# Kernel optimization log

Hardware: AMD Instinct MI355X
Metric: run time of the kernel (lower is better)

Reference implementation:

```python
import jax, jax.numpy as jnp
import numpy as np

B, S, D, H = 4, 2048, 1024, 16
DH = D // H


def setup_inputs() -> dict:
    key = jax.random.key(0)
    ks = jax.random.split(key, 12)
    std = 0.02
    return {
        "inputs": jax.random.normal(ks[0], (B, S, D), jnp.float32),
        "pre_block": jax.random.normal(ks[1], (B, S, D), jnp.float32),
        "ln_gamma": jnp.ones((D,), jnp.float32),
        "ln_beta": jnp.zeros((D,), jnp.float32),
        "Wq": jax.random.normal(ks[2], (D, D), jnp.float32) * std,
        "bq": jnp.zeros((D,), jnp.float32),
        "Wk": jax.random.normal(ks[3], (D, D), jnp.float32) * std,
        "bk": jnp.zeros((D,), jnp.float32),
        "Wv": jax.random.normal(ks[4], (D, D), jnp.float32) * std,
        "bv": jnp.zeros((D,), jnp.float32),
        "Wpos": jax.random.normal(ks[5], (D, D), jnp.float32) * std,
        "u_bias": jax.random.normal(ks[6], (H, DH), jnp.float32) * std,
        "v_bias": jax.random.normal(ks[7], (H, DH), jnp.float32) * std,
        "Wo": jax.random.normal(ks[8], (D, D), jnp.float32) * std,
        "bo": jnp.zeros((D,), jnp.float32),
    }


def _sinusoidal_pe(seq_len, d_model, dtype):
    pos = jnp.arange(seq_len, dtype=dtype)[:, None]                 # [S,1]
    i = jnp.arange(0, d_model, 2, dtype=dtype)
    div = jnp.exp(-(jnp.log(jnp.asarray(10000.0, dtype)) * i / d_model))  # [D/2]
    ang = pos * div                                                  # [S,D/2]
    pe = jnp.zeros((seq_len, d_model), dtype)
    pe = pe.at[:, 0::2].set(jnp.sin(ang)).at[:, 1::2].set(jnp.cos(ang))
    return pe


def _rel_shift(pos_score):
    # Transformer-XL style relative shift: pos_score [B,H,S,S]
    b, h, s1, s2 = pos_score.shape
    pad = jnp.zeros((b, h, s1, 1), pos_score.dtype)
    padded = jnp.concatenate([pad, pos_score], axis=-1)              # [B,H,S,S+1]
    padded = padded.reshape(b, h, s2 + 1, s1)
    return padded[:, :, 1:].reshape(b, h, s1, s2)


def _layer_norm(x, gamma, beta, eps=1e-5):
    mu = jnp.mean(x, axis=-1, keepdims=True)
    var = jnp.mean(jnp.square(x - mu), axis=-1, keepdims=True)
    return (x - mu) * jax.lax.rsqrt(var + eps) * gamma + beta


def reference(inputs, pre_block, ln_gamma, ln_beta, Wq, bq, Wk, bk, Wv, bv,
              Wpos, u_bias, v_bias, Wo, bo):
    b, s, d = inputs.shape
    h = u_bias.shape[0]
    dh = d // h

    pe = _sinusoidal_pe(s, d, inputs.dtype)                          # [S,D]
    x = _layer_norm(inputs, ln_gamma, ln_beta)

    q = (x @ Wq + bq).reshape(b, s, h, dh)
    k = (x @ Wk + bk).reshape(b, s, h, dh)
    v = (pre_block @ Wv + bv).reshape(b, s, h, dh)
    p = (pe @ Wpos).reshape(s, h, dh)                                # shared across batch

    content = jnp.einsum('bshd,bthd->bhst', q + u_bias, k)           # [B,H,S,S]
    pos_score = jnp.einsum('bshd,thd->bhst', q + v_bias, p)          # [B,H,S,S]
    pos_score = _rel_shift(pos_score)

    score = (content + pos_score) / jnp.sqrt(jnp.asarray(d, inputs.dtype))
    attn = jax.nn.softmax(score, axis=-1)
    ctx = jnp.einsum('bhst,bthd->bshd', attn, v).reshape(b, s, d)
    return ctx @ Wo + bo
```

## Files before the change

### kernel.cpp

```cpp
#include <hip/hip_runtime.h>
#include <hip/hip_bf16.h>
#include <cmath>

#define B_ 4
#define S_ 2048
#define D_ 1024
#define H_ 16
#define DH_ 64

typedef __attribute__((ext_vector_type(8))) short short8;
typedef __attribute__((ext_vector_type(4))) float f32x4;
#define MFMA_BF16(a, b, c) __builtin_amdgcn_mfma_f32_16x16x32_bf16(a, b, c, 0, 0, 0)

static __device__ __forceinline__ float b2f(unsigned short u) {
  union { unsigned int i; float f; } x; x.i = ((unsigned int)u) << 16; return x.f;
}
static __device__ __forceinline__ unsigned short f2b(float f) {
  union { float f; unsigned int i; } x; x.f = f;
  unsigned int r = x.i + 0x7FFFu + ((x.i >> 16) & 1u);
  return (unsigned short)(r >> 16);
}
static __device__ __forceinline__ unsigned int pk2(float a, float b) {
  __hip_bfloat162 h = __float22bfloat162_rn(make_float2(a, b));
  return *(unsigned int*)&h;
}
static __device__ __forceinline__ int mod96(int x) {
  int t = x >> 5;
  int q = (t * 43691) >> 17;
  int m3 = t - q * 3;
  return (x & 31) + (m3 << 5);
}
static __device__ __forceinline__ int clampS(int x) {
  return x < 0 ? 0 : (x > S_ - 1 ? S_ - 1 : x);
}
typedef __attribute__((address_space(3))) unsigned int lds_u32_t;
typedef __attribute__((address_space(1))) const unsigned int glb_u32_t;
static __device__ __forceinline__ void gload_lds16(const void* g, void* l) {
  __builtin_amdgcn_global_load_lds((glb_u32_t*)g, (lds_u32_t*)l, 16, 0, 0);
}

__global__ __launch_bounds__(256) void prep_kernel(
    const float* __restrict__ inputs, const float* __restrict__ gamma,
    const float* __restrict__ beta, unsigned short* __restrict__ xb,
    const float* __restrict__ pre, unsigned short* __restrict__ preb,
    const double* __restrict__ dt, unsigned short* __restrict__ pe,
    const float* __restrict__ Wq, unsigned short* __restrict__ wtq,
    const float* __restrict__ Wk, unsigned short* __restrict__ wtk,
    const float* __restrict__ Wv, unsigned short* __restrict__ wtv,
    const float* __restrict__ Wp, unsigned short* __restrict__ wtp,
    const float* __restrict__ Wo, unsigned short* __restrict__ wto) {
  __shared__ __align__(16) float shf[64 * 65];
  int bid = blockIdx.x;
  int tid = threadIdx.x;
  if (bid < 8192) {
    int row = bid;
    float4 val = ((const float4*)(inputs + (size_t)row * D_))[tid];
    float s = val.x + val.y + val.z + val.w;
    float sq = val.x * val.x + val.y * val.y + val.z * val.z + val.w * val.w;
#pragma unroll
    for (int o = 32; o > 0; o >>= 1) {
      s += __shfl_down(s, o);
      sq += __shfl_down(sq, o);
    }
    int wid = tid >> 6;
    if ((tid & 63) == 0) { shf[wid] = s; shf[4 + wid] = sq; }
    __syncthreads();
    if (tid == 0) {
      float ts = shf[0] + shf[1] + shf[2] + shf[3];
      float tq = shf[4] + shf[5] + shf[6] + shf[7];
      float mu = ts * (1.0f / D_);
      float var = tq * (1.0f / D_) - mu * mu;
      shf[8] = mu;
      shf[9] = rsqrtf(var + 1e-5f);
    }
    __syncthreads();
    float mu = shf[8], rs = shf[9];
    float4 g = ((const float4*)gamma)[tid];
    float4 be = ((const float4*)beta)[tid];
    ushort4 o;
    o.x = f2b((val.x - mu) * rs * g.x + be.x);
    o.y = f2b((val.y - mu) * rs * g.y + be.y);
    o.z = f2b((val.z - mu) * rs * g.z + be.z);
    o.w = f2b((val.w - mu) * rs * g.w + be.w);
    *(ushort4*)(xb + (size_t)row * D_ + tid * 4) = o;
    return;
  }
  bid -= 8192;
  if (bid < 8192) {
    size_t idx = (size_t)(bid * 256 + tid) * 4;
    float4 v = *(const float4*)(pre + idx);
    ushort4 o; o.x = f2b(v.x); o.y = f2b(v.y); o.z = f2b(v.z); o.w = f2b(v.w);
    *(ushort4*)(preb + idx) = o;
    return;
  }
  bid -= 8192;
  if (bid < 4096) {
    int idx = bid * 256 + tid;
    int t = idx >> 9;
    int i = idx & 511;
    double ang = (double)t * dt[i];
    double k = floor(ang * 0.15915494309189535);
    float red = (float)(ang - k * 6.283185307179586);
    ushort2 sc;
    sc.x = f2b(sinf(red));
    sc.y = f2b(cosf(red));
    *(ushort2*)(pe + (size_t)t * D_ + 2 * i) = sc;
    return;
  }
  bid -= 4096;
  const float* W; unsigned short* WT;
  switch (bid >> 8) {
    case 0: W = Wq; WT = wtq; break;
    case 1: W = Wk; WT = wtk; break;
    case 2: W = Wv; WT = wtv; break;
    case 3: W = Wp; WT = wtp; break;
    default: W = Wo; WT = wto; break;
  }
  int tile = bid & 255;
  int n0 = (tile & 15) * 64, k0 = (tile >> 4) * 64;
#pragma unroll
  for (int c = 0; c < 4; c++) {
    int idx = tid + c * 256;
    int r = idx >> 4;
    int ch = (idx & 15) * 4;
    float4 d = *(const float4*)(W + (size_t)(k0 + r) * D_ + n0 + ch);
    shf[r * 65 + ch] = d.x; shf[r * 65 + ch + 1] = d.y;
    shf[r * 65 + ch + 2] = d.z; shf[r * 65 + ch + 3] = d.w;
  }
  __syncthreads();
  {
    int n = tid >> 2;
    int ch = (tid & 3) * 16;
    unsigned short tmp[8];
#pragma unroll
    for (int half = 0; half < 2; half++) {
#pragma unroll
      for (int e = 0; e < 8; e++) tmp[e] = f2b(shf[(ch + half * 8 + e) * 65 + n]);
      *(short8*)(WT + (size_t)(n0 + n) * D_ + k0 + ch + half * 8) = *(short8*)tmp;
    }
  }
}

template <bool F32OUT>
__global__ __launch_bounds__(256) void gemm_bf16_t(const unsigned short* __restrict__ A,
                                                   const unsigned short* __restrict__ BT,
                                                   const float* __restrict__ bias,
                                                   void* __restrict__ Cv,
                                                   int M, int N, int K) {
  __shared__ __align__(16) unsigned short As[128 * 32];
  __shared__ __align__(16) unsigned short Bs[128 * 32];
  const int tid = threadIdx.x;
  const int wid = tid >> 6, lane = tid & 63, quad = lane >> 4, l15 = lane & 15;
  const int m0 = blockIdx.y * 128, n0 = blockIdx.x * 128;
  const int moff = (wid >> 1) * 64, noff = (wid & 1) * 64;
  f32x4 acc[4][4];
#pragma unroll
  for (int i = 0; i < 4; i++)
#pragma unroll
    for (int j = 0; j < 4; j++) acc[i][j] = (f32x4){0.f, 0.f, 0.f, 0.f};

  const int cb0 = wid * 64;
  const int c0 = cb0 + lane;
  const int r0 = c0 >> 2, ch0 = (c0 & 3) * 8;
  const int c1 = c0 + 256;
  const int r1 = c1 >> 2, ch1 = (c1 & 3) * 8;

  for (int k0 = 0; k0 < K; k0 += 32) {
    __syncthreads();
    gload_lds16(A + (size_t)(m0 + r0) * K + k0 + ch0, &As[cb0 * 8]);
    gload_lds16(BT + (size_t)(n0 + r0) * K + k0 + ch0, &Bs[cb0 * 8]);
    gload_lds16(A + (size_t)(m0 + r1) * K + k0 + ch1, &As[(cb0 + 256) * 8]);
    gload_lds16(BT + (size_t)(n0 + r1) * K + k0 + ch1, &Bs[(cb0 + 256) * 8]);
    __syncthreads();
    short8 af[4], bf[4];
#pragma unroll
    for (int i = 0; i < 4; i++)
      af[i] = *(const short8*)&As[(moff + i * 16 + l15) * 32 + quad * 8];
#pragma unroll
    for (int j = 0; j < 4; j++)
      bf[j] = *(const short8*)&Bs[(noff + j * 16 + l15) * 32 + quad * 8];
#pragma unroll
    for (int i = 0; i < 4; i++)
#pragma unroll
      for (int j = 0; j < 4; j++) acc[i][j] = MFMA_BF16(af[i], bf[j], acc[i][j]);
  }
#pragma unroll
  for (int i = 0; i < 4; i++) {
    int row = m0 + moff + i * 16 + quad * 4;
#pragma unroll
    for (int j = 0; j < 4; j++) {
      int col = n0 + noff + j * 16 + l15;
      float bb = bias ? bias[col] : 0.f;
#pragma unroll
      for (int g = 0; g < 4; g++) {
        if (F32OUT)
          ((float*)Cv)[(size_t)(row + g) * N + col] = acc[i][j][g] + bb;
        else
          ((unsigned short*)Cv)[(size_t)(row + g) * N + col] = f2b(acc[i][j][g] + bb);
      }
    }
  }
}

__global__ __launch_bounds__(256) void gemm_qk_bf16(const unsigned short* __restrict__ A,
                                                    const unsigned short* __restrict__ BT,
                                                    const float* __restrict__ bq,
                                                    const float* __restrict__ bk,
                                                    unsigned short* __restrict__ outQ,
                                                    unsigned short* __restrict__ outK) {
  const int K = D_;
  __shared__ __align__(16) unsigned short As[128 * 32];
  __shared__ __align__(16) unsigned short Bs[128 * 32];
  const int tid = threadIdx.x;
  const int wid = tid >> 6, lane = tid & 63, quad = lane >> 4, l15 = lane & 15;
  const int m0 = blockIdx.y * 128, n0 = blockIdx.x * 128;
  const int moff = (wid >> 1) * 64, noff = (wid & 1) * 64;
  f32x4 acc[4][4];
#pragma unroll
  for (int i = 0; i < 4; i++)
#pragma unroll
    for (int j = 0; j < 4; j++) acc[i][j] = (f32x4){0.f, 0.f, 0.f, 0.f};

  const int cb0 = wid * 64;
  const int c0 = cb0 + lane;
  const int r0 = c0 >> 2, ch0 = (c0 & 3) * 8;
  const int c1 = c0 + 256;
  const int r1 = c1 >> 2, ch1 = (c1 & 3) * 8;

  for (int k0 = 0; k0 < K; k0 += 32) {
    __syncthreads();
    gload_lds16(A + (size_t)(m0 + r0) * K + k0 + ch0, &As[cb0 * 8]);
    gload_lds16(BT + (size_t)(n0 + r0) * K + k0 + ch0, &Bs[cb0 * 8]);
    gload_lds16(A + (size_t)(m0 + r1) * K + k0 + ch1, &As[(cb0 + 256) * 8]);
    gload_lds16(BT + (size_t)(n0 + r1) * K + k0 + ch1, &Bs[(cb0 + 256) * 8]);
    __syncthreads();
    short8 af[4], bf[4];
#pragma unroll
    for (int i = 0; i < 4; i++)
      af[i] = *(const short8*)&As[(moff + i * 16 + l15) * 32 + quad * 8];
#pragma unroll
    for (int j = 0; j < 4; j++)
      bf[j] = *(const short8*)&Bs[(noff + j * 16 + l15) * 32 + quad * 8];
#pragma unroll
    for (int i = 0; i < 4; i++)
#pragma unroll
      for (int j = 0; j < 4; j++) acc[i][j] = MFMA_BF16(af[i], bf[j], acc[i][j]);
  }
  const float* bias = (n0 < D_) ? bq : bk;
  unsigned short* outp = (n0 < D_) ? outQ : outK;
  const int nn0 = n0 & (D_ - 1);
#pragma unroll
  for (int i = 0; i < 4; i++) {
    int row = m0 + moff + i * 16 + quad * 4;
#pragma unroll
    for (int j = 0; j < 4; j++) {
      int col = nn0 + noff + j * 16 + l15;
      float bb = bias[col];
#pragma unroll
      for (int g = 0; g < 4; g++)
        outp[(size_t)(row + g) * D_ + col] = f2b(acc[i][j][g] + bb);
    }
  }
}

__global__ __launch_bounds__(256) void post_kernel(const unsigned short* __restrict__ v,
                                                   unsigned short* __restrict__ vt,
                                                   const unsigned short* __restrict__ p,
                                                   const float* __restrict__ ub,
                                                   const float* __restrict__ vbb,
                                                   float* __restrict__ cw) {
  __shared__ __align__(16) unsigned short t[64 * 72];
  int bid = blockIdx.x;
  int tid = threadIdx.x;
  if (bid < 2048) {
    int s0 = (bid & 31) * 64, h = (bid >> 5) & 15, b = bid >> 9;
#pragma unroll
    for (int c = 0; c < 2; c++) {
      int idx = tid + c * 256;
      int r = idx >> 3, ch = (idx & 7) * 8;
      short8 d = *(const short8*)(v + (((size_t)b * S_ + s0 + r) * H_ + h) * DH_ + ch);
      *(short8*)&t[r * 72 + ch] = d;
    }
    __syncthreads();
    int dh = tid >> 2, ch = tid & 3;
    unsigned short tmp[8];
#pragma unroll
    for (int half = 0; half < 2; half++) {
#pragma unroll
      for (int e = 0; e < 8; e++) tmp[e] = t[(ch * 16 + half * 8 + e) * 72 + dh];
      *(short8*)(vt + ((size_t)(b * H_ + h) * 64 + dh) * S_ + s0 + ch * 16 + half * 8) =
          *(short8*)tmp;
    }
    return;
  }
  int idx = (bid - 2048) * 256 + tid;
  int r = idx & (S_ - 1), h = idx >> 11;
  float s = 0.f;
#pragma unroll 8
  for (int c = 0; c < 64; c++)
    s += (vbb[h * 64 + c] - ub[h * 64 + c]) * b2f(p[(size_t)r * D_ + h * 64 + c]);
  cw[idx] = s;
}

__global__ __launch_bounds__(256) void attn_kernel(const unsigned short* __restrict__ q,
                                                   const unsigned short* __restrict__ kg,
                                                   const unsigned short* __restrict__ vtg,
                                                   const unsigned short* __restrict__ pg,
                                                   const float* __restrict__ ub,
                                                   const float* __restrict__ cw,
                                                   unsigned short* __restrict__ ctx) {
  int flat = blockIdx.x + 32 * (blockIdx.y + 16 * blockIdx.z);
  int swz = (flat & 7) * 256 + (flat >> 3);
  const int i0 = (swz & 31) * 64;
  const int h = (swz >> 5) & 15;
  const int b = swz >> 9;
  const int tid = threadIdx.x;
  const int wid = tid >> 6, lane = tid & 63, quad = lane >> 4, l15 = lane & 15;
  const int wr0 = wid * 16;
  const int ib = i0 >> 5;

  __shared__ __align__(16) unsigned short ks[32 * 64];
  __shared__ __align__(16) unsigned short ps[2][32 * 64];
  __shared__ __align__(16) unsigned short vts[2][64 * 32];
  __shared__ __align__(16) unsigned short prb[64 * 40];
  __shared__ __align__(16) unsigned short bandA[64 * 100];
  __shared__ __align__(16) unsigned short bandB[64 * 100];

  const int srow = tid >> 3;
  const int lcS = ((tid & 7) ^ (srow & 7)) * 8;
  const int vrow = tid >> 2, vch = (tid & 3) * 8;
  const int pc0 = (quad ^ (l15 & 7)) * 8;

  const unsigned short* kgl = kg + ((size_t)b * S_ * H_ + h) * DH_ + lcS;
  const unsigned short* pgl = pg + h * 64 + lcS;
  const unsigned short* vgl = vtg + ((size_t)(b * H_ + h) * 64 + vrow) * S_ + vch;
  const float* cwh = cw + h * S_;
  const int wb = wid * 512;

  short8 qa00, qa01, qa10, qa11;
  {
    auto ldq = [&](int r, int c0) -> short8 {
      int qi = i0 + r; if (qi > S_ - 1) qi = S_ - 1;
      short8 raw = *(const short8*)(q + (((size_t)b * S_ + qi) * H_ + h) * DH_ + c0);
      unsigned short t[8];
#pragma unroll
      for (int e = 0; e < 8; e++)
        t[e] = f2b(b2f((unsigned short)raw[e]) + ub[h * 64 + c0 + e]);
      return *(short8*)t;
    };
    qa00 = ldq(wr0 + l15, quad * 8);
    qa01 = ldq(wr0 + l15, 32 + quad * 8);
    qa10 = ldq(wr0 + l15 + 1, quad * 8);
    qa11 = ldq(wr0 + l15 + 1, 32 + quad * 8);
  }

  const int brow = (wr0 + l15) * 100;

  auto band_compute = [&](const unsigned short* src, int w, int rhi) {
    int rbase = rhi - 31;
    short8 a0 = w ? qa10 : qa00;
    short8 a1 = w ? qa11 : qa01;
    unsigned short* band = w ? bandB : bandA;
    const int OFF = w ? 2 : 1;
#pragma unroll
    for (int ct = 0; ct < 2; ct++) {
      int ro = (ct * 16 + l15) * 64;
      short8 b0 = *(const short8*)&src[ro + pc0];
      short8 b1 = *(const short8*)&src[ro + (pc0 ^ 32)];
      f32x4 acc = (f32x4){0.f, 0.f, 0.f, 0.f};
      acc = MFMA_BF16(b0, a0, acc);
      acc = MFMA_BF16(b1, a1, acc);
      int r0 = rbase + ct * 16 + quad * 4;
      float c0 = cwh[clampS(r0)];
      float c1 = cwh[clampS(r0 + 1)];
      float c2 = cwh[clampS(r0 + 2)];
      float c3 = cwh[clampS(r0 + 3)];
      int col = mod96(r0 + 960 + OFF);
      uint2 pv = make_uint2(pk2(acc[0] + c0, acc[1] + c1), pk2(acc[2] + c2, acc[3] + c3));
      *(uint2*)&band[brow + col] = pv;
      if (col == 0) *(uint2*)&band[brow + 96] = pv;
    }
  };

  {
    const int TW[5] = {0, 0, 0, 1, 1};
    const int TR[5] = {S_ + 30 - i0 - 64, S_ + 30 - i0 - 32, S_ + 30 - i0, 29, 61};
    {
      int rc = clampS(TR[0] - 31 + srow);
      gload_lds16(pgl + (size_t)rc * D_, &ps[0][wb]);
      gload_lds16(kgl + (size_t)srow * (H_ * DH_), &ks[wb]);
      gload_lds16(vgl, &vts[0][wb]);
    }
    __syncthreads();
#pragma unroll
    for (int t = 0; t < 5; t++) {
      if (t < 4) {
        int rc = clampS(TR[t + 1] - 31 + srow);
        gload_lds16(pgl + (size_t)rc * D_, &ps[(t + 1) & 1][wb]);
      }
      band_compute(ps[t & 1], TW[t], TR[t]);
      __syncthreads();
    }
  }

  float lsum = 0.f;
  f32x4 Oa[4];
#pragma unroll
  for (int ct = 0; ct < 4; ct++) Oa[ct] = (f32x4){0.f, 0.f, 0.f, 0.f};

  int cA = mod96(S_ + quad * 4 - i0 - wr0 - l15);
  int cB = mod96(2112 + quad * 4 - i0 - wr0 - l15);
  int cwin = 0, crhi = 0, chave = 0;

  const float SCL = 0.03125f;
  const unsigned int prbw = (wr0 + l15) * 40 + quad * 4;

  for (int jt = 0; jt < 64; jt++) {
    const int j0 = jt * 32;
    const int cur = jt & 1, nxt = cur ^ 1;
    int pwin = 0, prhi = 0, havep = 0;
    {
      int j0x = j0 + 32;
      if (j0x <= i0 + 63) { pwin = 0; prhi = S_ + 30 - i0 + j0x; havep = 1; }
      else if (jt < 63)   { pwin = 1; prhi = j0x - i0 + 29;      havep = 1; }
      if (havep) {
        int rc = clampS(prhi - 31 + srow);
        gload_lds16(pgl + (size_t)rc * D_, &ps[nxt][wb]);
      }
      if (jt < 63)
        gload_lds16(vgl + (size_t)(j0 + 32), &vts[nxt][wb]);
    }
    if (chave) band_compute(ps[cur], cwin, crhi);
    f32x4 cc[2];
    {
#pragma unroll
      for (int ct = 0; ct < 2; ct++) {
        int ro = (ct * 16 + l15) * 64;
        short8 a0 = *(const short8*)&ks[ro + pc0];
        short8 a1 = *(const short8*)&ks[ro + (pc0 ^ 32)];
        f32x4 acc = (f32x4){0.f, 0.f, 0.f, 0.f};
        acc = MFMA_BF16(a0, qa00, acc);
        acc = MFMA_BF16(a1, qa01, acc);
        cc[ct] = acc;
      }
    }
    __syncthreads();
    if (jt < 63)
      gload_lds16(kgl + (size_t)(j0 + 32 + srow) * (H_ * DH_), &ks[wb]);
    if (jt < ib) {
#pragma unroll
      for (int ct = 0; ct < 2; ct++) {
        int c0 = ct ? (cA + 16 >= 96 ? cA + 16 - 96 : cA + 16) : cA;
        const unsigned short* base = &bandA[brow + c0];
        float e0 = __expf((cc[ct][0] + b2f(base[0])) * SCL);
        float e1 = __expf((cc[ct][1] + b2f(base[1])) * SCL);
        float e2 = __expf((cc[ct][2] + b2f(base[2])) * SCL);
        float e3 = __expf((cc[ct][3] + b2f(base[3])) * SCL);
        *(uint2*)&prb[prbw + ct * 16] = make_uint2(pk2(e0, e1), pk2(e2, e3));
        lsum += (e0 + e1) + (e2 + e3);
      }
    } else if (jt >= ib + 3) {
#pragma unroll
      for (int ct = 0; ct < 2; ct++) {
        int c0 = ct ? (cB + 16 >= 96 ? cB + 16 - 96 : cB + 16) : cB;
        const unsigned short* base = &bandB[brow + c0];
        float e0 = __expf((cc[ct][0] + b2f(base[0])) * SCL);
        float e1 = __expf((cc[ct][1] + b2f(base[1])) * SCL);
        float e2 = __expf((cc[ct][2] + b2f(base[2])) * SCL);
        float e3 = __expf((cc[ct][3] + b2f(base[3])) * SCL);
        *(uint2*)&prb[prbw + ct * 16] = make_uint2(pk2(e0, e1), pk2(e2, e3));
        lsum += (e0 + e1) + (e2 + e3);
      }
    } else {
#pragma unroll
      for (int ct = 0; ct < 2; ct++) {
        int jbase = j0 + ct * 16 + quad * 4;
        float ev[4];
#pragma unroll
        for (int g = 0; g < 4; g++) {
          int d = jbase + g - (i0 + wr0 + l15);
          float t;
          if (d == 1) t = 0.f;
          else if (d <= 0) t = b2f(bandA[brow + mod96(S_ + d)]);
          else t = b2f(bandB[brow + mod96(d)]);
          ev[g] = __expf((cc[ct][g] + t) * SCL);
          lsum += ev[g];
        }
        *(uint2*)&prb[prbw + ct * 16] = make_uint2(pk2(ev[0], ev[1]), pk2(ev[2], ev[3]));
      }
    }
    {
      short8 af = *(const short8*)&prb[(wr0 + l15) * 40 + quad * 8];
#pragma unroll
      for (int ct = 0; ct < 4; ct++) {
        short8 bf = *(const short8*)&vts[cur][(ct * 16 + l15) * 32 + quad * 8];
        Oa[ct] = MFMA_BF16(af, bf, Oa[ct]);
      }
    }
    __syncthreads();
    cwin = pwin; crhi = prhi; chave = havep;
    cA += 32; if (cA >= 96) cA -= 96;
    cB += 32; if (cB >= 96) cB -= 96;
  }
  float ltot = lsum;
  ltot += __shfl_xor(ltot, 16);
  ltot += __shfl_xor(ltot, 32);
#pragma unroll
  for (int g = 0; g < 4; g++) {
    float lg = __shfl(ltot, quad * 4 + g);
    float inv = 1.f / lg;
    int i = i0 + wr0 + quad * 4 + g;
    unsigned short* dst = ctx + ((size_t)b * S_ + i) * D_ + h * 64;
#pragma unroll
    for (int ct = 0; ct < 4; ct++) dst[ct * 16 + l15] = f2b(Oa[ct][g] * inv);
  }
}

extern "C" void kernel_launch(void* const* d_in, const int* in_sizes, int n_in,
                              void* d_out, int out_size, void* d_ws, size_t ws_size,
                              hipStream_t stream) {
  const float* inputs = (const float*)d_in[0];
  const float* pre_block = (const float*)d_in[1];
  const float* ln_gamma = (const float*)d_in[2];
  const float* ln_beta = (const float*)d_in[3];
  const float* Wq = (const float*)d_in[4];
  const float* bq = (const float*)d_in[5];
  const float* Wk = (const float*)d_in[6];
  const float* bk = (const float*)d_in[7];
  const float* Wv = (const float*)d_in[8];
  const float* bv = (const float*)d_in[9];
  const float* Wpos = (const float*)d_in[10];
  const float* u_bias = (const float*)d_in[11];
  const float* v_bias = (const float*)d_in[12];
  const float* Wo = (const float*)d_in[13];
  const float* bo = (const float*)d_in[14];
  float* out = (float*)d_out;

  char* ws = (char*)d_ws;
  const size_t NBS = (size_t)B_ * S_ * D_;
  unsigned short* xb = (unsigned short*)ws;
  unsigned short* ctx = (unsigned short*)ws;
  unsigned short* preb = (unsigned short*)(ws + NBS * 2);
  unsigned short* peb = (unsigned short*)(ws + NBS * 4);
  char* base = ws + NBS * 4 + (size_t)S_ * D_ * 2;
  unsigned short* wtq = (unsigned short*)(base);
  unsigned short* wtk = (unsigned short*)(base + (size_t)D_ * D_ * 2);
  unsigned short* wtv = (unsigned short*)(base + (size_t)D_ * D_ * 4);
  unsigned short* wtp = (unsigned short*)(base + (size_t)D_ * D_ * 6);
  unsigned short* wto = (unsigned short*)(base + (size_t)D_ * D_ * 8);
  unsigned short* qb = (unsigned short*)(base + (size_t)D_ * D_ * 10);
  unsigned short* kb = qb + NBS;
  unsigned short* vb = kb + NBS;
  unsigned short* vtb = vb + NBS;
  unsigned short* pb = vtb + NBS;
  float* cww = (float*)(pb + (size_t)S_ * D_);
  double* divtab = (double*)(cww + (size_t)H_ * S_);

  static double h_divtab[512];
  static bool h_init = false;
  if (!h_init) {
    for (int i = 0; i < 512; i++)
      h_divtab[i] = exp(-(log(10000.0) * (2.0 * i) / (double)D_));
    h_init = true;
  }
  hipMemcpyAsync(divtab, h_divtab, 512 * sizeof(double), hipMemcpyHostToDevice, stream);

  prep_kernel<<<21760, 256, 0, stream>>>(inputs, ln_gamma, ln_beta, xb,
                                         pre_block, preb, divtab, peb,
                                         Wq, wtq, Wk, wtk, Wv, wtv, Wpos, wtp, Wo, wto);
  gemm_qk_bf16<<<dim3(16, 64), 256, 0, stream>>>(xb, wtq, bq, bk, qb, kb);
  gemm_bf16_t<false><<<dim3(8, 64), 256, 0, stream>>>(preb, wtv, bv, vb, B_ * S_, D_, D_);
  gemm_bf16_t<false><<<dim3(8, 16), 256, 0, stream>>>(peb, wtp, nullptr, pb, S_, D_, D_);
  post_kernel<<<2176, 256, 0, stream>>>(vb, vtb, pb, u_bias, v_bias, cww);
  attn_kernel<<<dim3(32, 16, 4), 256, 0, stream>>>(qb, kb, vtb, pb, u_bias, cww, ctx);
  gemm_bf16_t<true><<<dim3(8, 64), 256, 0, stream>>>(ctx, wto, bo, out, B_ * S_, D_, D_);
}
```

Before: 635.1 us.

## Fold v_bias into a separate query copy instead of precomputed positional correction

Previously the query was biased by u_bias for both the content and positional MFMAs, and a correction term (v_bias-u_bias)·p was precomputed per head and row in post_kernel, then loaded and added in the band computation. Now the attention kernel keeps separate q+u_bias and q+v_bias register copies and uses the latter for the positional band, so the correction buffer, its computation blocks and its gathered loads go away. This costs extra registers for the additional query fragments. It also raises wave priority around the MFMA section with s_setprio.

```diff
diff --git a/kernel.cpp b/kernel.cpp
--- a/kernel.cpp
+++ b/kernel.cpp
@@ -264,42 +264,28 @@
 }
 
 __global__ __launch_bounds__(256) void post_kernel(const unsigned short* __restrict__ v,
-                                                   unsigned short* __restrict__ vt,
-                                                   const unsigned short* __restrict__ p,
-                                                   const float* __restrict__ ub,
-                                                   const float* __restrict__ vbb,
-                                                   float* __restrict__ cw) {
+                                                   unsigned short* __restrict__ vt) {
   __shared__ __align__(16) unsigned short t[64 * 72];
   int bid = blockIdx.x;
   int tid = threadIdx.x;
-  if (bid < 2048) {
-    int s0 = (bid & 31) * 64, h = (bid >> 5) & 15, b = bid >> 9;
-#pragma unroll
-    for (int c = 0; c < 2; c++) {
-      int idx = tid + c * 256;
-      int r = idx >> 3, ch = (idx & 7) * 8;
-      short8 d = *(const short8*)(v + (((size_t)b * S_ + s0 + r) * H_ + h) * DH_ + ch);
-      *(short8*)&t[r * 72 + ch] = d;
-    }
-    __syncthreads();
-    int dh = tid >> 2, ch = tid & 3;
-    unsigned short tmp[8];
-#pragma unroll
-    for (int half = 0; half < 2; half++) {
-#pragma unroll
-      for (int e = 0; e < 8; e++) tmp[e] = t[(ch * 16 + half * 8 + e) * 72 + dh];
-      *(short8*)(vt + ((size_t)(b * H_ + h) * 64 + dh) * S_ + s0 + ch * 16 + half * 8) =
-          *(short8*)tmp;
-    }
-    return;
-  }
-  int idx = (bid - 2048) * 256 + tid;
-  int r = idx & (S_ - 1), h = idx >> 11;
-  float s = 0.f;
-#pragma unroll 8
-  for (int c = 0; c < 64; c++)
-    s += (vbb[h * 64 + c] - ub[h * 64 + c]) * b2f(p[(size_t)r * D_ + h * 64 + c]);
-  cw[idx] = s;
+  int s0 = (bid & 31) * 64, h = (bid >> 5) & 15, b = bid >> 9;
+#pragma unroll
+  for (int c = 0; c < 2; c++) {
+    int idx = tid + c * 256;
+    int r = idx >> 3, ch = (idx & 7) * 8;
+    short8 d = *(const short8*)(v + (((size_t)b * S_ + s0 + r) * H_ + h) * DH_ + ch);
+    *(short8*)&t[r * 72 + ch] = d;
+  }
+  __syncthreads();
+  int dh = tid >> 2, ch = tid & 3;
+  unsigned short tmp[8];
+#pragma unroll
+  for (int half = 0; half < 2; half++) {
+#pragma unroll
+    for (int e = 0; e < 8; e++) tmp[e] = t[(ch * 16 + half * 8 + e) * 72 + dh];
+    *(short8*)(vt + ((size_t)(b * H_ + h) * 64 + dh) * S_ + s0 + ch * 16 + half * 8) =
+        *(short8*)tmp;
+  }
 }
 
 __global__ __launch_bounds__(256) void attn_kernel(const unsigned short* __restrict__ q,
@@ -307,7 +293,7 @@
                                                    const unsigned short* __restrict__ vtg,
                                                    const unsigned short* __restrict__ pg,
                                                    const float* __restrict__ ub,
-                                                   const float* __restrict__ cw,
+                                                   const float* __restrict__ vbias,
                                                    unsigned short* __restrict__ ctx) {
   int flat = blockIdx.x + 32 * (blockIdx.y + 16 * blockIdx.z);
   int swz = (flat & 7) * 256 + (flat >> 3);
@@ -334,32 +320,44 @@
   const unsigned short* kgl = kg + ((size_t)b * S_ * H_ + h) * DH_ + lcS;
   const unsigned short* pgl = pg + h * 64 + lcS;
   const unsigned short* vgl = vtg + ((size_t)(b * H_ + h) * 64 + vrow) * S_ + vch;
-  const float* cwh = cw + h * S_;
   const int wb = wid * 512;
 
-  short8 qa00, qa01, qa10, qa11;
+  short8 qc0, qc1, qA0, qA1, qB0, qB1;
   {
-    auto ldq = [&](int r, int c0) -> short8 {
+    auto ldq2 = [&](int r, int c0, short8& outU, short8& outV) {
       int qi = i0 + r; if (qi > S_ - 1) qi = S_ - 1;
       short8 raw = *(const short8*)(q + (((size_t)b * S_ + qi) * H_ + h) * DH_ + c0);
-      unsigned short t[8];
+      unsigned short tu[8], tv[8];
+#pragma unroll
+      for (int e = 0; e < 8; e++) {
+        float f = b2f((unsigned short)raw[e]);
+        tu[e] = f2b(f + ub[h * 64 + c0 + e]);
+        tv[e] = f2b(f + vbias[h * 64 + c0 + e]);
+      }
+      outU = *(short8*)tu;
+      outV = *(short8*)tv;
+    };
+    auto ldqv = [&](int r, int c0) -> short8 {
+      int qi = i0 + r; if (qi > S_ - 1) qi = S_ - 1;
+      short8 raw = *(const short8*)(q + (((size_t)b * S_ + qi) * H_ + h) * DH_ + c0);
+      unsigned short tv[8];
 #pragma unroll
       for (int e = 0; e < 8; e++)
-        t[e] = f2b(b2f((unsigned short)raw[e]) + ub[h * 64 + c0 + e]);
-      return *(short8*)t;
+        tv[e] = f2b(b2f((unsigned short)raw[e]) + vbias[h * 64 + c0 + e]);
+      return *(short8*)tv;
     };
-    qa00 = ldq(wr0 + l15, quad * 8);
-    qa01 = ldq(wr0 + l15, 32 + quad * 8);
-    qa10 = ldq(wr0 + l15 + 1, quad * 8);
-    qa11 = ldq(wr0 + l15 + 1, 32 + quad * 8);
+    ldq2(wr0 + l15, quad * 8, qc0, qA0);
+    ldq2(wr0 + l15, 32 + quad * 8, qc1, qA1);
+    qB0 = ldqv(wr0 + l15 + 1, quad * 8);
+    qB1 = ldqv(wr0 + l15 + 1, 32 + quad * 8);
   }
 
   const int brow = (wr0 + l15) * 100;
 
   auto band_compute = [&](const unsigned short* src, int w, int rhi) {
     int rbase = rhi - 31;
-    short8 a0 = w ? qa10 : qa00;
-    short8 a1 = w ? qa11 : qa01;
+    short8 a0 = w ? qB0 : qA0;
+    short8 a1 = w ? qB1 : qA1;
     unsigned short* band = w ? bandB : bandA;
     const int OFF = w ? 2 : 1;
 #pragma unroll
@@ -371,12 +369,8 @@
       acc = MFMA_BF16(b0, a0, acc);
       acc = MFMA_BF16(b1, a1, acc);
       int r0 = rbase + ct * 16 + quad * 4;
-      float c0 = cwh[clampS(r0)];
-      float c1 = cwh[clampS(r0 + 1)];
-      float c2 = cwh[clampS(r0 + 2)];
-      float c3 = cwh[clampS(r0 + 3)];
       int col = mod96(r0 + 960 + OFF);
-      uint2 pv = make_uint2(pk2(acc[0] + c0, acc[1] + c1), pk2(acc[2] + c2, acc[3] + c3));
+      uint2 pv = make_uint2(pk2(acc[0], acc[1]), pk2(acc[2], acc[3]));
       *(uint2*)&band[brow + col] = pv;
       if (col == 0) *(uint2*)&band[brow + 96] = pv;
     }
@@ -430,6 +424,7 @@
       if (jt < 63)
         gload_lds16(vgl + (size_t)(j0 + 32), &vts[nxt][wb]);
     }
+    __builtin_amdgcn_s_setprio(1);
     if (chave) band_compute(ps[cur], cwin, crhi);
     f32x4 cc[2];
     {
@@ -439,11 +434,12 @@
         short8 a0 = *(const short8*)&ks[ro + pc0];
         short8 a1 = *(const short8*)&ks[ro + (pc0 ^ 32)];
         f32x4 acc = (f32x4){0.f, 0.f, 0.f, 0.f};
-        acc = MFMA_BF16(a0, qa00, acc);
-        acc = MFMA_BF16(a1, qa01, acc);
+        acc = MFMA_BF16(a0, qc0, acc);
+        acc = MFMA_BF16(a1, qc1, acc);
         cc[ct] = acc;
       }
     }
+    __builtin_amdgcn_s_setprio(0);
     __syncthreads();
     if (jt < 63)
       gload_lds16(kgl + (size_t)(j0 + 32 + srow) * (H_ * DH_), &ks[wb]);
@@ -553,8 +549,7 @@
   unsigned short* vb = kb + NBS;
   unsigned short* vtb = vb + NBS;
   unsigned short* pb = vtb + NBS;
-  float* cww = (float*)(pb + (size_t)S_ * D_);
-  double* divtab = (double*)(cww + (size_t)H_ * S_);
+  double* divtab = (double*)(pb + (size_t)S_ * D_);
 
   static double h_divtab[512];
   static bool h_init = false;
@@ -571,7 +566,7 @@
   gemm_qk_bf16<<<dim3(16, 64), 256, 0, stream>>>(xb, wtq, bq, bk, qb, kb);
   gemm_bf16_t<false><<<dim3(8, 64), 256, 0, stream>>>(preb, wtv, bv, vb, B_ * S_, D_, D_);
   gemm_bf16_t<false><<<dim3(8, 16), 256, 0, stream>>>(peb, wtp, nullptr, pb, S_, D_, D_);
-  post_kernel<<<2176, 256, 0, stream>>>(vb, vtb, pb, u_bias, v_bias, cww);
-  attn_kernel<<<dim3(32, 16, 4), 256, 0, stream>>>(qb, kb, vtb, pb, u_bias, cww, ctx);
+  post_kernel<<<2048, 256, 0, stream>>>(vb, vtb);
+  attn_kernel<<<dim3(32, 16, 4), 256, 0, stream>>>(qb, kb, vtb, pb, u_bias, v_bias, ctx);
   gemm_bf16_t<true><<<dim3(8, 64), 256, 0, stream>>>(ctx, wto, bo, out, B_ * S_, D_, D_);
 }
```

Result: faster. 614.6 us (-3.2%).
